# Kernel tuning notes

Hardware: AMD Instinct MI355X
Metric: run time of the kernel (lower is better)

## Reference

```python
import jax, jax.numpy as jnp
import numpy as np


def setup_inputs() -> dict:
    H = 2048          # code_size == decoder_size (required for output feedback)
    T = 512           # sentence_length
    key = jax.random.key(0)
    k = jax.random.split(key, 5)
    s = 1.0 / np.sqrt(H)  # PyTorch LSTM init range
    return {
        "X": jax.random.normal(k[0], (1, 1, H), dtype=jnp.float32),
        "W_ih": jax.random.uniform(k[1], (4 * H, H), jnp.float32, -s, s),
        "W_hh": jax.random.uniform(k[2], (4 * H, H), jnp.float32, -s, s),
        "b_ih": jax.random.uniform(k[3], (4 * H,), jnp.float32, -s, s),
        "b_hh": jax.random.uniform(k[4], (4 * H,), jnp.float32, -s, s),
        "sentence_length": T,
    }


def reference(X, W_ih, W_hh, b_ih, b_hh, sentence_length):
    # the previous output h. PyTorch gate order: i, f, g, o.
    H = W_hh.shape[1]
    x0 = X[0]                       # (1, H)  batch=1
    h0 = jnp.zeros((1, H), X.dtype)
    c0 = jnp.zeros((1, H), X.dtype)

    def step(carry, _):
        x, h, c = carry
        gates = x @ W_ih.T + b_ih + h @ W_hh.T + b_hh   # (1, 4H)
        i, f, g, o = jnp.split(gates, 4, axis=-1)
        c_new = jax.nn.sigmoid(f) * c + jax.nn.sigmoid(i) * jnp.tanh(g)
        h_new = jax.nn.sigmoid(o) * jnp.tanh(c_new)
        # next step's input is this step's output (decoder feedback)
        return (h_new, h_new, c_new), h_new

    _, ys = jax.lax.scan(step, (x0, h0, c0), None, length=sentence_length)
    return ys  # (T, 1, H) == torch all_output
```

## Files before the change

### kernel.cpp

```cpp
#include <hip/hip_runtime.h>
#include <hip/hip_fp16.h>
#include <math.h>

#define HDIM 2048
#define G4   (4 * HDIM)
#define NBLK 256
#define TPB  512
#define NSLOT 1024

typedef __fp16 h2_t __attribute__((ext_vector_type(2)));

__device__ __forceinline__ float fast_sigmoid(float x) {
    return 1.0f / (1.0f + __expf(-x));
}
__device__ __forceinline__ float fast_tanh(float x) {
    return 1.0f - 2.0f / (1.0f + __expf(2.0f * x));
}
__device__ __forceinline__ h2_t pk2(float a, float b) {
#if __has_builtin(__builtin_amdgcn_cvt_pkrtz)
    return __builtin_amdgcn_cvt_pkrtz(a, b);
#else
    return h2_t{(__fp16)a, (__fp16)b};
#endif
}

__global__ __launch_bounds__(256) void prep_slots(unsigned long long* __restrict__ slots) {
    int i = blockIdx.x * blockDim.x + threadIdx.x;
    if (i < 2 * NSLOT) slots[i] = 0ull;
}

__global__ __launch_bounds__(256) void prep_small(const float* __restrict__ bih,
                                                  const float* __restrict__ bhh,
                                                  float* __restrict__ bsum,
                                                  float* __restrict__ c) {
    int i = blockIdx.x * blockDim.x + threadIdx.x;
    if (i < G4) bsum[i] = bih[i] + bhh[i];
    if (i < HDIM) c[i] = 0.0f;
}

__global__ __launch_bounds__(256) void prep_wsum_h(const float* __restrict__ Wih,
                                                   const float* __restrict__ Whh,
                                                   __half* __restrict__ Wsum) {
    const int n8 = (G4 * HDIM) / 8;
    int idx = blockIdx.x * blockDim.x + threadIdx.x;
    int stride = gridDim.x * blockDim.x;
    const float4* a = (const float4*)Wih;
    const float4* b = (const float4*)Whh;
    for (int i = idx; i < n8; i += stride) {
        float4 a0 = a[2 * i], a1 = a[2 * i + 1];
        float4 b0 = b[2 * i], b1 = b[2 * i + 1];
        __half h[8];
        h[0] = __float2half(a0.x + b0.x);
        h[1] = __float2half(a0.y + b0.y);
        h[2] = __float2half(a0.z + b0.z);
        h[3] = __float2half(a0.w + b0.w);
        h[4] = __float2half(a1.x + b1.x);
        h[5] = __float2half(a1.y + b1.y);
        h[6] = __float2half(a1.z + b1.z);
        h[7] = __float2half(a1.w + b1.w);
        ((uint4*)Wsum)[i] = *(const uint4*)h;
    }
}

__global__ __launch_bounds__(256) void lstm_step_f32(const float* __restrict__ x,
                                                     const float* __restrict__ W,
                                                     const float* __restrict__ bsum,
                                                     float* __restrict__ c,
                                                     float* __restrict__ h_out) {
    __shared__ float gates[4][8];
    const int tid  = threadIdx.x;
    const int wave = tid >> 6;
    const int lane = tid & 63;
    const int j0   = blockIdx.x * 8;

    float4 xv[8];
    const float4* xp = (const float4*)x;
#pragma unroll
    for (int k = 0; k < 8; ++k) xv[k] = xp[lane + 64 * k];

    float acc[8];
#pragma unroll
    for (int j8 = 0; j8 < 8; ++j8) {
        const int R = wave * HDIM + j0 + j8;
        const float4* wr = (const float4*)(W + (size_t)R * HDIM);
        float a = 0.0f;
#pragma unroll
        for (int k = 0; k < 8; ++k) {
            float4 wv = wr[lane + 64 * k];
            a += wv.x * xv[k].x + wv.y * xv[k].y + wv.z * xv[k].z + wv.w * xv[k].w;
        }
        acc[j8] = a;
    }
#pragma unroll
    for (int j8 = 0; j8 < 8; ++j8) {
        float a = acc[j8];
#pragma unroll
        for (int off = 32; off > 0; off >>= 1) a += __shfl_down(a, off, 64);
        if (lane == 0) gates[wave][j8] = a + bsum[wave * HDIM + j0 + j8];
    }
    __syncthreads();
    if (tid < 8) {
        const int j = j0 + tid;
        const float si = 1.0f / (1.0f + expf(-gates[0][tid]));
        const float so = 1.0f / (1.0f + expf(-gates[3][tid]));
        const float tg = tanhf(gates[2][tid]);
        const float cn = si * tg;
        c[j]     = cn;
        h_out[j] = so * tanhf(cn);
    }
}

__global__ __launch_bounds__(256) void lstm_step_h(const float* __restrict__ x,
                                                   const __half* __restrict__ W,
                                                   const float* __restrict__ bsum,
                                                   float* __restrict__ c,
                                                   float* __restrict__ h_out) {
    __shared__ float gates[4][8];
    const int tid  = threadIdx.x;
    const int wave = tid >> 6;
    const int lane = tid & 63;
    const int j0   = blockIdx.x * 8;

    float xv[32];
    const float4* xp = (const float4*)x;
#pragma unroll
    for (int k = 0; k < 4; ++k) {
        float4 a = xp[k * 128 + lane * 2];
        float4 b = xp[k * 128 + lane * 2 + 1];
        xv[k * 8 + 0] = a.x; xv[k * 8 + 1] = a.y; xv[k * 8 + 2] = a.z; xv[k * 8 + 3] = a.w;
        xv[k * 8 + 4] = b.x; xv[k * 8 + 5] = b.y; xv[k * 8 + 6] = b.z; xv[k * 8 + 7] = b.w;
    }
    float acc[8];
#pragma unroll
    for (int j8 = 0; j8 < 8; ++j8) {
        const int R = wave * HDIM + j0 + j8;
        const uint4* wr = (const uint4*)(W + (size_t)R * HDIM);
        float a = 0.0f;
#pragma unroll
        for (int k = 0; k < 4; ++k) {
            uint4 wv = wr[k * 64 + lane];
            const __half* hh = (const __half*)&wv;
#pragma unroll
            for (int e = 0; e < 8; ++e)
                a = fmaf(__half2float(hh[e]), xv[k * 8 + e], a);
        }
        acc[j8] = a;
    }
#pragma unroll
    for (int j8 = 0; j8 < 8; ++j8) {
        float a = acc[j8];
#pragma unroll
        for (int off = 32; off > 0; off >>= 1) a += __shfl_down(a, off, 64);
        if (lane == 0) gates[wave][j8] = a + bsum[wave * HDIM + j0 + j8];
    }
    __syncthreads();
    if (tid < 8) {
        const int j = j0 + tid;
        const float si = 1.0f / (1.0f + expf(-gates[0][tid]));
        const float sf = 1.0f / (1.0f + expf(-gates[1][tid]));
        const float so = 1.0f / (1.0f + expf(-gates[3][tid]));
        const float tg = tanhf(gates[2][tid]);
        const float cn = sf * c[j] + si * tg;
        c[j]     = cn;
        h_out[j] = so * tanhf(cn);
    }
}

__global__ __launch_bounds__(TPB, 2) void lstm_persist(const float* __restrict__ X,
                                                       const float* __restrict__ Wih,
                                                       const float* __restrict__ Whh,
                                                       const float* __restrict__ bih,
                                                       const float* __restrict__ bhh,
                                                       float* __restrict__ out,
                                                       unsigned long long* __restrict__ slots,
                                                       int T) {
    const int tid  = threadIdx.x;
    const int wave = tid >> 6;
    const int lane = tid & 63;
    const int jH   = blockIdx.x * 8 + wave;

    if (wave == 0) __builtin_amdgcn_s_setprio(1);

    float xv[32];
    {
        const float4* xp = (const float4*)X;
#pragma unroll
        for (int e = 0; e < 4; ++e) {
            float4 a = xp[(lane + 64 * e) * 2];
            float4 b = xp[(lane + 64 * e) * 2 + 1];
            xv[e * 8 + 0] = a.x; xv[e * 8 + 1] = a.y; xv[e * 8 + 2] = a.z; xv[e * 8 + 3] = a.w;
            xv[e * 8 + 4] = b.x; xv[e * 8 + 5] = b.y; xv[e * 8 + 6] = b.z; xv[e * 8 + 7] = b.w;
        }
    }

    uint4 w[4][4];
    float bias[4], acc[4];
#pragma unroll
    for (int g = 0; g < 4; ++g) {
        const size_t R = (size_t)g * HDIM + jH;
        const float4* ri = (const float4*)(Wih + R * HDIM);
        const float4* rh = (const float4*)(Whh + R * HDIM);
        float a0acc = 0.0f;
#pragma unroll
        for (int e = 0; e < 4; ++e) {
            float4 a0 = ri[(lane + 64 * e) * 2];
            float4 a1 = ri[(lane + 64 * e) * 2 + 1];
            float4 b0 = rh[(lane + 64 * e) * 2];
            float4 b1 = rh[(lane + 64 * e) * 2 + 1];
            a0acc += a0.x * xv[e * 8 + 0] + a0.y * xv[e * 8 + 1]
                   + a0.z * xv[e * 8 + 2] + a0.w * xv[e * 8 + 3]
                   + a1.x * xv[e * 8 + 4] + a1.y * xv[e * 8 + 5]
                   + a1.z * xv[e * 8 + 6] + a1.w * xv[e * 8 + 7];
            h2_t p0 = pk2(a0.x + b0.x, a0.y + b0.y);
            h2_t p1 = pk2(a0.z + b0.z, a0.w + b0.w);
            h2_t p2 = pk2(a1.x + b1.x, a1.y + b1.y);
            h2_t p3 = pk2(a1.z + b1.z, a1.w + b1.w);
            w[g][e] = make_uint4(__builtin_bit_cast(unsigned, p0),
                                 __builtin_bit_cast(unsigned, p1),
                                 __builtin_bit_cast(unsigned, p2),
                                 __builtin_bit_cast(unsigned, p3));
        }
        acc[g]  = a0acc;
        bias[g] = bih[R] + bhh[R];
    }

    __shared__ __align__(16) unsigned lds_x[2][NSLOT];
    __shared__ unsigned short h16[8];
    __shared__ float h_outf[8];

    float cc = 0.0f;

#pragma unroll
    for (int g = 0; g < 4; ++g)
#pragma unroll
        for (int off = 32; off > 0; off >>= 1)
            acc[g] += __shfl_xor(acc[g], off, 64);
    {
        const float si = fast_sigmoid(acc[0] + bias[0]);
        const float tg = fast_tanh(acc[2] + bias[2]);
        const float so = fast_sigmoid(acc[3] + bias[3]);
        cc = si * tg;
        const float h = so * fast_tanh(cc);
        if (lane == 0) {
            h16[wave] = (unsigned short)(__builtin_bit_cast(unsigned, pk2(h, h)) & 0xffffu);
            h_outf[wave] = h;
        }
    }
    __syncthreads();
    if (wave == 0 && lane < 4) {
        const unsigned payload = (unsigned)h16[2 * lane]
                               | ((unsigned)h16[2 * lane + 1] << 16);
        unsigned long long pkv = (1ull << 32) | (unsigned long long)payload;
        __hip_atomic_store(&slots[blockIdx.x * 4 + lane], pkv,
                           __ATOMIC_RELAXED, __HIP_MEMORY_SCOPE_AGENT);
    }

    for (int t = 1; t < T; ++t) {
        if (wave == 1 && lane < 8) {
            out[(size_t)(t - 1) * HDIM + blockIdx.x * 8 + lane] = h_outf[lane];
        }

        const int buf = (t - 1) & 1;
        const unsigned long long* sl = slots + (size_t)buf * NSLOT;
        const unsigned tg = (unsigned)t;
        const int s0 = tid;
        const int s1 = tid + 512;

        unsigned long long v0 = __hip_atomic_load(&sl[s0], __ATOMIC_RELAXED,
                                                  __HIP_MEMORY_SCOPE_AGENT);
        unsigned long long v1 = __hip_atomic_load(&sl[s1], __ATOMIC_RELAXED,
                                                  __HIP_MEMORY_SCOPE_AGENT);
        int spin = 0;
        while (((unsigned)(v0 >> 32) != tg) | ((unsigned)(v1 >> 32) != tg)) {
            if (spin++) __builtin_amdgcn_s_sleep(1);
            if ((unsigned)(v0 >> 32) != tg)
                v0 = __hip_atomic_load(&sl[s0], __ATOMIC_RELAXED,
                                       __HIP_MEMORY_SCOPE_AGENT);
            if ((unsigned)(v1 >> 32) != tg)
                v1 = __hip_atomic_load(&sl[s1], __ATOMIC_RELAXED,
                                       __HIP_MEMORY_SCOPE_AGENT);
        }
        lds_x[buf][s0] = (unsigned)v0;
        lds_x[buf][s1] = (unsigned)v1;
        __syncthreads();

        float a2[4] = {0.f, 0.f, 0.f, 0.f};
#pragma unroll
        for (int e = 0; e < 4; ++e) {
            const uint4 xq = *(const uint4*)&lds_x[buf][(lane + 64 * e) * 4];
            const unsigned xs[4] = {xq.x, xq.y, xq.z, xq.w};
#pragma unroll
            for (int p = 0; p < 4; ++p) {
                const h2_t xh = __builtin_bit_cast(h2_t, xs[p]);
#pragma unroll
                for (int g = 0; g < 4; ++g) {
                    const h2_t* wh = (const h2_t*)&w[g][e];
#if __has_builtin(__builtin_amdgcn_fdot2)
                    a2[g] = __builtin_amdgcn_fdot2(wh[p], xh, a2[g], false);
#else
                    a2[g] = fmaf((float)wh[p][0], (float)xh[0],
                                 fmaf((float)wh[p][1], (float)xh[1], a2[g]));
#endif
                }
            }
        }

#pragma unroll
        for (int g = 0; g < 4; ++g)
#pragma unroll
            for (int off = 32; off > 0; off >>= 1)
                a2[g] += __shfl_xor(a2[g], off, 64);

        const float si = fast_sigmoid(a2[0] + bias[0]);
        const float sf = fast_sigmoid(a2[1] + bias[1]);
        const float tg2 = fast_tanh(a2[2] + bias[2]);
        const float so = fast_sigmoid(a2[3] + bias[3]);
        cc = sf * cc + si * tg2;
        const float h = so * fast_tanh(cc);

        if (lane == 0) {
            h16[wave] = (unsigned short)(__builtin_bit_cast(unsigned, pk2(h, h)) & 0xffffu);
            h_outf[wave] = h;
        }
        __syncthreads();

        if (wave == 0 && lane < 4) {
            const unsigned payload = (unsigned)h16[2 * lane]
                                   | ((unsigned)h16[2 * lane + 1] << 16);
            unsigned long long pkv = ((unsigned long long)(unsigned)(t + 1) << 32)
                                   | (unsigned long long)payload;
            __hip_atomic_store(&slots[(size_t)(t & 1) * NSLOT + blockIdx.x * 4 + lane],
                               pkv, __ATOMIC_RELAXED, __HIP_MEMORY_SCOPE_AGENT);
        }
    }

    if (wave == 1 && lane < 8) {
        out[(size_t)(T - 1) * HDIM + blockIdx.x * 8 + lane] = h_outf[lane];
    }
}

extern "C" void kernel_launch(void* const* d_in, const int* in_sizes, int n_in,
                              void* d_out, int out_size, void* d_ws, size_t ws_size,
                              hipStream_t stream) {
    const float* X   = (const float*)d_in[0];
    const float* Wih = (const float*)d_in[1];
    const float* Whh = (const float*)d_in[2];
    const float* bih = (const float*)d_in[3];
    const float* bhh = (const float*)d_in[4];
    float* out = (float*)d_out;

    int T = out_size / HDIM;

    const size_t wsum_bytes = (size_t)G4 * HDIM * sizeof(__half);
    char* ws = (char*)d_ws;
    __half* Wsum = (__half*)ws;
    float*  bsum = (float*)(ws + wsum_bytes);
    float*  c    = bsum + G4;
    unsigned long long* slots = (unsigned long long*)(c + HDIM);

    prep_slots<<<8, 256, 0, stream>>>(slots);

    void* args[] = {(void*)&X, (void*)&Wih, (void*)&Whh, (void*)&bih,
                    (void*)&bhh, (void*)&out, (void*)&slots, (void*)&T};
    hipError_t err = hipLaunchCooperativeKernel((const void*)lstm_persist,
                                                dim3(NBLK), dim3(TPB), args, 0, stream);
    if (err != hipSuccess) {
        prep_small<<<(G4 + 255) / 256, 256, 0, stream>>>(bih, bhh, bsum, c);
        prep_wsum_h<<<2048, 256, 0, stream>>>(Wih, Whh, Wsum);
        lstm_step_f32<<<256, 256, 0, stream>>>(X, Wih, bsum, c, out);
        for (int t = 1; t < T; ++t) {
            const float* hprev = out + (size_t)(t - 1) * HDIM;
            float* hnext = out + (size_t)t * HDIM;
            lstm_step_h<<<256, 256, 0, stream>>>(hprev, Wsum, bsum, c, hnext);
        }
    }
}
```

Before: 1.511 ms.

## Publish per-wave 32-bit tagged slots and drop the per-step block barrier

Each wave now writes its own fp16 hidden value plus a 16-bit step tag straight to a 32-bit global slot. Before, lane 0 of every wave staged its value in shared memory, the block hit a second __syncthreads, and wave 0 packed pairs into 64-bit slots. Removing that barrier and staging hop shortens the per-step critical path. Readers now poll four 32-bit words per thread instead of two 64-bit words, which raises polling traffic. The output staging buffer is double-buffered to stay race-free without the barrier, and the wave-priority boost is removed.

New measurement: 3.568 ms. +136.2%, slower.

```diff
diff --git a/kernel.cpp b/kernel.cpp
--- a/kernel.cpp
+++ b/kernel.cpp
@@ -6,7 +6,7 @@
 #define G4   (4 * HDIM)
 #define NBLK 256
 #define TPB  512
-#define NSLOT 1024
+#define NWORD 2048
 
 typedef __fp16 h2_t __attribute__((ext_vector_type(2)));
 
@@ -24,9 +24,13 @@
 #endif
 }
 
-__global__ __launch_bounds__(256) void prep_slots(unsigned long long* __restrict__ slots) {
+__device__ __forceinline__ unsigned wld(const unsigned* p) {
+    return __hip_atomic_load(p, __ATOMIC_RELAXED, __HIP_MEMORY_SCOPE_AGENT);
+}
+
+__global__ __launch_bounds__(256) void prep_slots(unsigned* __restrict__ slots) {
     int i = blockIdx.x * blockDim.x + threadIdx.x;
-    if (i < 2 * NSLOT) slots[i] = 0ull;
+    if (i < 2 * NWORD) slots[i] = 0u;
 }
 
 __global__ __launch_bounds__(256) void prep_small(const float* __restrict__ bih,
@@ -172,14 +176,13 @@
                                                        const float* __restrict__ bih,
                                                        const float* __restrict__ bhh,
                                                        float* __restrict__ out,
-                                                       unsigned long long* __restrict__ slots,
+                                                       unsigned* __restrict__ slots,
                                                        int T) {
     const int tid  = threadIdx.x;
     const int wave = tid >> 6;
     const int lane = tid & 63;
     const int jH   = blockIdx.x * 8 + wave;
-
-    if (wave == 0) __builtin_amdgcn_s_setprio(1);
+    const int myword = blockIdx.x * 8 + wave;
 
     float xv[32];
     {
@@ -224,9 +227,8 @@
         bias[g] = bih[R] + bhh[R];
     }
 
-    __shared__ __align__(16) unsigned lds_x[2][NSLOT];
-    __shared__ unsigned short h16[8];
-    __shared__ float h_outf[8];
+    __shared__ __align__(16) unsigned lds_x[2][NWORD / 2];
+    __shared__ float h_outf[2][8];
 
     float cc = 0.0f;
 
@@ -242,47 +244,36 @@
         cc = si * tg;
         const float h = so * fast_tanh(cc);
         if (lane == 0) {
-            h16[wave] = (unsigned short)(__builtin_bit_cast(unsigned, pk2(h, h)) & 0xffffu);
-            h_outf[wave] = h;
-        }
-    }
-    __syncthreads();
-    if (wave == 0 && lane < 4) {
-        const unsigned payload = (unsigned)h16[2 * lane]
-                               | ((unsigned)h16[2 * lane + 1] << 16);
-        unsigned long long pkv = (1ull << 32) | (unsigned long long)payload;
-        __hip_atomic_store(&slots[blockIdx.x * 4 + lane], pkv,
-                           __ATOMIC_RELAXED, __HIP_MEMORY_SCOPE_AGENT);
+            const unsigned h16 = __builtin_bit_cast(unsigned, pk2(h, h)) & 0xffffu;
+            __hip_atomic_store(&slots[myword], (1u << 16) | h16,
+                               __ATOMIC_RELAXED, __HIP_MEMORY_SCOPE_AGENT);
+            h_outf[0][wave] = h;
+        }
     }
 
     for (int t = 1; t < T; ++t) {
+        const int buf = (t - 1) & 1;
+        const unsigned* sl = slots + (size_t)buf * NWORD + 4 * (size_t)tid;
+        const unsigned tg = (unsigned)t;
+
+        unsigned v0 = wld(sl + 0), v1 = wld(sl + 1), v2 = wld(sl + 2), v3 = wld(sl + 3);
+        int spin = 0;
+        while (((v0 >> 16) != tg) | ((v1 >> 16) != tg) |
+               ((v2 >> 16) != tg) | ((v3 >> 16) != tg)) {
+            if (spin++) __builtin_amdgcn_s_sleep(1);
+            if ((v0 >> 16) != tg) v0 = wld(sl + 0);
+            if ((v1 >> 16) != tg) v1 = wld(sl + 1);
+            if ((v2 >> 16) != tg) v2 = wld(sl + 2);
+            if ((v3 >> 16) != tg) v3 = wld(sl + 3);
+        }
+        lds_x[buf][2 * tid]     = (v0 & 0xffffu) | (v1 << 16);
+        lds_x[buf][2 * tid + 1] = (v2 & 0xffffu) | (v3 << 16);
+        __syncthreads();
+
         if (wave == 1 && lane < 8) {
-            out[(size_t)(t - 1) * HDIM + blockIdx.x * 8 + lane] = h_outf[lane];
-        }
-
-        const int buf = (t - 1) & 1;
-        const unsigned long long* sl = slots + (size_t)buf * NSLOT;
-        const unsigned tg = (unsigned)t;
-        const int s0 = tid;
-        const int s1 = tid + 512;
-
-        unsigned long long v0 = __hip_atomic_load(&sl[s0], __ATOMIC_RELAXED,
-                                                  __HIP_MEMORY_SCOPE_AGENT);
-        unsigned long long v1 = __hip_atomic_load(&sl[s1], __ATOMIC_RELAXED,
-                                                  __HIP_MEMORY_SCOPE_AGENT);
-        int spin = 0;
-        while (((unsigned)(v0 >> 32) != tg) | ((unsigned)(v1 >> 32) != tg)) {
-            if (spin++) __builtin_amdgcn_s_sleep(1);
-            if ((unsigned)(v0 >> 32) != tg)
-                v0 = __hip_atomic_load(&sl[s0], __ATOMIC_RELAXED,
-                                       __HIP_MEMORY_SCOPE_AGENT);
-            if ((unsigned)(v1 >> 32) != tg)
-                v1 = __hip_atomic_load(&sl[s1], __ATOMIC_RELAXED,
-                                       __HIP_MEMORY_SCOPE_AGENT);
-        }
-        lds_x[buf][s0] = (unsigned)v0;
-        lds_x[buf][s1] = (unsigned)v1;
-        __syncthreads();
+            out[(size_t)(t - 1) * HDIM + blockIdx.x * 8 + lane] =
+                h_outf[(t - 1) & 1][lane];
+        }
 
         float a2[4] = {0.f, 0.f, 0.f, 0.f};
 #pragma unroll
@@ -319,23 +310,18 @@
         const float h = so * fast_tanh(cc);
 
         if (lane == 0) {
-            h16[wave] = (unsigned short)(__builtin_bit_cast(unsigned, pk2(h, h)) & 0xffffu);
-            h_outf[wave] = h;
-        }
-        __syncthreads();
-
-        if (wave == 0 && lane < 4) {
-            const unsigned payload = (unsigned)h16[2 * lane]
-                                   | ((unsigned)h16[2 * lane + 1] << 16);
-            unsigned long long pkv = ((unsigned long long)(unsigned)(t + 1) << 32)
-                                   | (unsigned long long)payload;
-            __hip_atomic_store(&slots[(size_t)(t & 1) * NSLOT + blockIdx.x * 4 + lane],
-                               pkv, __ATOMIC_RELAXED, __HIP_MEMORY_SCOPE_AGENT);
-        }
-    }
-
+            const unsigned h16 = __builtin_bit_cast(unsigned, pk2(h, h)) & 0xffffu;
+            __hip_atomic_store(&slots[(size_t)(t & 1) * NWORD + myword],
+                               ((unsigned)(t + 1) << 16) | h16,
+                               __ATOMIC_RELAXED, __HIP_MEMORY_SCOPE_AGENT);
+            h_outf[t & 1][wave] = h;
+        }
+    }
+
+    __syncthreads();
     if (wave == 1 && lane < 8) {
-        out[(size_t)(T - 1) * HDIM + blockIdx.x * 8 + lane] = h_outf[lane];
+        out[(size_t)(T - 1) * HDIM + blockIdx.x * 8 + lane] =
+            h_outf[(T - 1) & 1][lane];
     }
 }
 
@@ -356,9 +342,9 @@
     __half* Wsum = (__half*)ws;
     float*  bsum = (float*)(ws + wsum_bytes);
     float*  c    = bsum + G4;
-    unsigned long long* slots = (unsigned long long*)(c + HDIM);
-
-    prep_slots<<<8, 256, 0, stream>>>(slots);
+    unsigned* slots = (unsigned*)(c + HDIM);
+
+    prep_slots<<<16, 256, 0, stream>>>(slots);
 
     void* args[] = {(void*)&X, (void*)&Wih, (void*)&Whh, (void*)&bih,
                     (void*)&bhh, (void*)&out, (void*)&slots, (void*)&T};
```

## Replace per-step barrier with LDS tag flags and transpose-style gate reduction

Applied to the files above, without the earlier changes.

Removes the second __syncthreads per timestep. Each wave publishes its h value into a double-buffered LDS slot tagged with the step number, and wave 0 spins on those tags before writing the global slot. The four per-gate butterfly reductions are merged into one interleaved reduction, so each lane ends up owning one gate and evaluates a single sigmoid, with tanh written as 2*sigmoid(2x)-1. The output store moves after the remaining barrier and reads from a double-buffered h_outf. This shortens the serial critical path, but it relies on LDS spin-waits with relaxed ordering and on the 16-bit tag not wrapping within the tested T.

Result: no change. 1.535 ms (+1.6%).

```diff
diff --git a/kernel.cpp b/kernel.cpp
--- a/kernel.cpp
+++ b/kernel.cpp
@@ -179,6 +179,12 @@
     const int lane = tid & 63;
     const int jH   = blockIdx.x * 8 + wave;
 
+    __shared__ __align__(16) unsigned lds_x[2][NSLOT];
+    __shared__ unsigned h_sig[2][8];
+    __shared__ float h_outf[2][8];
+
+    if (tid < 16) ((unsigned*)h_sig)[tid] = 0u;
+
     if (wave == 0) __builtin_amdgcn_s_setprio(1);
 
     float xv[32];
@@ -224,42 +230,57 @@
         bias[g] = bih[R] + bhh[R];
     }
 
-    __shared__ __align__(16) unsigned lds_x[2][NSLOT];
-    __shared__ unsigned short h16[8];
-    __shared__ float h_outf[8];
+    __syncthreads();
+
+    const float bias_g = (lane & 2) ? ((lane & 1) ? bias[3] : bias[2])
+                                    : ((lane & 1) ? bias[1] : bias[0]);
+    const bool  isg    = ((lane & 3) == 2);
+    const int   bse    = lane & ~3;
 
     float cc = 0.0f;
 
-#pragma unroll
-    for (int g = 0; g < 4; ++g)
-#pragma unroll
-        for (int off = 32; off > 0; off >>= 1)
-            acc[g] += __shfl_xor(acc[g], off, 64);
     {
-        const float si = fast_sigmoid(acc[0] + bias[0]);
-        const float tg = fast_tanh(acc[2] + bias[2]);
-        const float so = fast_sigmoid(acc[3] + bias[3]);
-        cc = si * tg;
-        const float h = so * fast_tanh(cc);
+        float z01 = (lane & 1) ? acc[1] : acc[0];
+        float u01 = (lane & 1) ? acc[0] : acc[1];
+        z01 += __shfl_xor(u01, 1, 64);
+        float z23 = (lane & 1) ? acc[3] : acc[2];
+        float u23 = (lane & 1) ? acc[2] : acc[3];
+        z23 += __shfl_xor(u23, 1, 64);
+        float y = (lane & 2) ? z23 : z01;
+        float v = (lane & 2) ? z01 : z23;
+        y += __shfl_xor(v, 2, 64);
+#pragma unroll
+        for (int off = 4; off < 64; off <<= 1) y += __shfl_xor(y, off, 64);
+
+        const float s   = y + bias_g;
+        const float arg = isg ? 2.0f * s : s;
+        const float sg  = fast_sigmoid(arg);
+        const float act = isg ? 2.0f * sg - 1.0f : sg;
+        const float gi = __shfl(act, bse + 0, 64);
+        const float gg = __shfl(act, bse + 2, 64);
+        const float go = __shfl(act, bse + 3, 64);
+        cc = gi * gg;
+        const float h = go * fast_tanh(cc);
         if (lane == 0) {
-            h16[wave] = (unsigned short)(__builtin_bit_cast(unsigned, pk2(h, h)) & 0xffffu);
-            h_outf[wave] = h;
-        }
-    }
-    __syncthreads();
-    if (wave == 0 && lane < 4) {
-        const unsigned payload = (unsigned)h16[2 * lane]
-                               | ((unsigned)h16[2 * lane + 1] << 16);
-        unsigned long long pkv = (1ull << 32) | (unsigned long long)payload;
-        __hip_atomic_store(&slots[blockIdx.x * 4 + lane], pkv,
-                           __ATOMIC_RELAXED, __HIP_MEMORY_SCOPE_AGENT);
+            const unsigned h16v = __builtin_bit_cast(unsigned, pk2(h, h)) & 0xffffu;
+            __hip_atomic_store(&h_sig[0][wave], (1u << 16) | h16v,
+                               __ATOMIC_RELAXED, __HIP_MEMORY_SCOPE_WORKGROUP);
+            h_outf[0][wave] = h;
+        }
+        if (wave == 0 && lane < 4) {
+            unsigned va, vb;
+            do { va = __hip_atomic_load(&h_sig[0][2 * lane], __ATOMIC_RELAXED,
+                                        __HIP_MEMORY_SCOPE_WORKGROUP); } while ((va >> 16) != 1u);
+            do { vb = __hip_atomic_load(&h_sig[0][2 * lane + 1], __ATOMIC_RELAXED,
+                                        __HIP_MEMORY_SCOPE_WORKGROUP); } while ((vb >> 16) != 1u);
+            const unsigned payload = (va & 0xffffu) | (vb << 16);
+            unsigned long long pkv = (1ull << 32) | (unsigned long long)payload;
+            __hip_atomic_store(&slots[blockIdx.x * 4 + lane], pkv,
+                               __ATOMIC_RELAXED, __HIP_MEMORY_SCOPE_AGENT);
+        }
     }
 
     for (int t = 1; t < T; ++t) {
-        if (wave == 1 && lane < 8) {
-            out[(size_t)(t - 1) * HDIM + blockIdx.x * 8 + lane] = h_outf[lane];
-        }
-
         const int buf = (t - 1) & 1;
         const unsigned long long* sl = slots + (size_t)buf * NSLOT;
         const unsigned tg = (unsigned)t;
@@ -284,6 +305,11 @@
         lds_x[buf][s1] = (unsigned)v1;
         __syncthreads();
 
+        if (wave == 1 && lane < 8) {
+            out[(size_t)(t - 1) * HDIM + blockIdx.x * 8 + lane] =
+                h_outf[(t - 1) & 1][lane];
+        }
+
         float a2[4] = {0.f, 0.f, 0.f, 0.f};
 #pragma unroll
         for (int e = 0; e < 4; ++e) {
@@ -305,37 +331,56 @@
             }
         }
 
-#pragma unroll
-        for (int g = 0; g < 4; ++g)
-#pragma unroll
-            for (int off = 32; off > 0; off >>= 1)
-                a2[g] += __shfl_xor(a2[g], off, 64);
-
-        const float si = fast_sigmoid(a2[0] + bias[0]);
-        const float sf = fast_sigmoid(a2[1] + bias[1]);
-        const float tg2 = fast_tanh(a2[2] + bias[2]);
-        const float so = fast_sigmoid(a2[3] + bias[3]);
-        cc = sf * cc + si * tg2;
-        const float h = so * fast_tanh(cc);
+        float z01 = (lane & 1) ? a2[1] : a2[0];
+        float u01 = (lane & 1) ? a2[0] : a2[1];
+        z01 += __shfl_xor(u01, 1, 64);
+        float z23 = (lane & 1) ? a2[3] : a2[2];
+        float u23 = (lane & 1) ? a2[2] : a2[3];
+        z23 += __shfl_xor(u23, 1, 64);
+        float y = (lane & 2) ? z23 : z01;
+        float v = (lane & 2) ? z01 : z23;
+        y += __shfl_xor(v, 2, 64);
+#pragma unroll
+        for (int off = 4; off < 64; off <<= 1) y += __shfl_xor(y, off, 64);
+
+        const float s   = y + bias_g;
+        const float arg = isg ? 2.0f * s : s;
+        const float sg  = fast_sigmoid(arg);
+        const float act = isg ? 2.0f * sg - 1.0f : sg;
+        const float gi = __shfl(act, bse + 0, 64);
+        const float gf = __shfl(act, bse + 1, 64);
+        const float gg = __shfl(act, bse + 2, 64);
+        const float go = __shfl(act, bse + 3, 64);
+        cc = gf * cc + gi * gg;
+        const float h = go * fast_tanh(cc);
 
         if (lane == 0) {
-            h16[wave] = (unsigned short)(__builtin_bit_cast(unsigned, pk2(h, h)) & 0xffffu);
-            h_outf[wave] = h;
-        }
-        __syncthreads();
+            const unsigned h16v = __builtin_bit_cast(unsigned, pk2(h, h)) & 0xffffu;
+            __hip_atomic_store(&h_sig[t & 1][wave],
+                               ((unsigned)(t + 1) << 16) | h16v,
+                               __ATOMIC_RELAXED, __HIP_MEMORY_SCOPE_WORKGROUP);
+            h_outf[t & 1][wave] = h;
+        }
 
         if (wave == 0 && lane < 4) {
-            const unsigned payload = (unsigned)h16[2 * lane]
-                                   | ((unsigned)h16[2 * lane + 1] << 16);
-            unsigned long long pkv = ((unsigned long long)(unsigned)(t + 1) << 32)
+            const unsigned tagv = (unsigned)(t + 1);
+            unsigned va, vb;
+            do { va = __hip_atomic_load(&h_sig[t & 1][2 * lane], __ATOMIC_RELAXED,
+                                        __HIP_MEMORY_SCOPE_WORKGROUP); } while ((va >> 16) != tagv);
+            do { vb = __hip_atomic_load(&h_sig[t & 1][2 * lane + 1], __ATOMIC_RELAXED,
+                                        __HIP_MEMORY_SCOPE_WORKGROUP); } while ((vb >> 16) != tagv);
+            const unsigned payload = (va & 0xffffu) | (vb << 16);
+            unsigned long long pkv = ((unsigned long long)tagv << 32)
                                    | (unsigned long long)payload;
             __hip_atomic_store(&slots[(size_t)(t & 1) * NSLOT + blockIdx.x * 4 + lane],
                                pkv, __ATOMIC_RELAXED, __HIP_MEMORY_SCOPE_AGENT);
         }
     }
 
+    __syncthreads();
     if (wave == 1 && lane < 8) {
-        out[(size_t)(T - 1) * HDIM + blockIdx.x * 8 + lane] = h_outf[lane];
+        out[(size_t)(T - 1) * HDIM + blockIdx.x * 8 + lane] =
+            h_outf[(T - 1) & 1][lane];
     }
 }
 
```
